# Performance work log

Measured on AMD Instinct MI355X. Metric: run time of the kernel, lower is better.

Reference implementation:

```python
import jax, jax.numpy as jnp
import numpy as np

B, T, C, H = 8, 2048, 1024, 128

def setup_inputs() -> dict:
    key = jax.random.key(0)
    k1, k2, k3, k4 = jax.random.split(key, 4)
    scale = 0.02
    return {
        "x": jax.random.normal(k1, (B, T, C), dtype=jnp.float32),
        "Wq": jax.random.normal(k2, (C, H), dtype=jnp.float32) * scale,
        "Wk": jax.random.normal(k3, (C, H), dtype=jnp.float32) * scale,
        "Wv": jax.random.normal(k4, (C, H), dtype=jnp.float32) * scale,
    }

def reference(x, Wq, Wk, Wv):
    # Single causal attention head (dropout p=0.0 -> identity)
    q = jnp.einsum('btc,ch->bth', x, Wq)
    k = jnp.einsum('btc,ch->bth', x, Wk)
    v = jnp.einsum('btc,ch->bth', x, Wv)
    head_size = k.shape[-1]
    scores = jnp.einsum('bth,bsh->bts', q, k) / jnp.sqrt(jnp.asarray(head_size, q.dtype))  # [B,T,T]
    causal = jnp.tril(jnp.ones((scores.shape[1], scores.shape[2]), dtype=bool))
    scores = jnp.where(causal, scores, -jnp.inf)
    weights = jax.nn.softmax(scores, axis=-1)
    context = jnp.einsum('bts,bsh->bth', weights, v)  # [B,T,H]
    return context
```

## Files before the change

### kernel.cpp

```cpp
#include <hip/hip_runtime.h>

typedef __bf16 bf16x8 __attribute__((ext_vector_type(8)));
typedef float f32x4 __attribute__((ext_vector_type(4)));
typedef float fv4 __attribute__((ext_vector_type(4)));

#define B_ 8
#define T_ 2048
#define C_ 1024
#define H_ 128

__global__ __launch_bounds__(256) void prep_kernel(
    const float* __restrict__ Wq, const float* __restrict__ Wk,
    const float* __restrict__ Wv, __bf16* __restrict__ Wt)
{
  __shared__ __bf16 ldsT[128 * 136];
  const int tid = threadIdx.x;
  const int k0 = blockIdx.x * 128;
  const int wsel = blockIdx.y;
  const float* W = wsel == 0 ? Wq : (wsel == 1 ? Wk : Wv);
#pragma unroll
  for (int i = 0; i < 16; ++i) {
    int fidx = tid + 256 * i;
    int k = fidx >> 5, h4 = (fidx & 31) << 2;
    fv4 w = *(const fv4*)(W + (size_t)(k0 + k) * H_ + h4);
#pragma unroll
    for (int j = 0; j < 4; ++j) ldsT[(h4 + j) * 136 + k] = (__bf16)w[j];
  }
  __syncthreads();
#pragma unroll
  for (int i = 0; i < 8; ++i) {
    int sidx = tid + 256 * i;
    int h = sidx >> 4, c8 = (sidx & 15) << 3;
    *(bf16x8*)(Wt + (size_t)wsel * H_ * C_ + (size_t)h * C_ + k0 + c8) =
        *(const bf16x8*)&ldsT[h * 136 + c8];
  }
}

__global__ __launch_bounds__(256) void proj_kernel(
    const float* __restrict__ x, const __bf16* __restrict__ Wt,
    __bf16* __restrict__ Qw, __bf16* __restrict__ Kw, __bf16* __restrict__ Vtw)
{
  __shared__ __align__(16) __bf16 ldsA[32 * 40];
  __shared__ __align__(16) __bf16 ldsB[384 * 40];
  const int tid = threadIdx.x;
  const int wave = tid >> 6, lane = tid & 63;
  const int q4 = lane >> 4, l16 = lane & 15;
  const int bt0 = blockIdx.x * 32;

  const f32x4 zero4 = {0.f, 0.f, 0.f, 0.f};
  f32x4 acc[2][6];
#pragma unroll
  for (int mt = 0; mt < 2; ++mt)
#pragma unroll
    for (int nt = 0; nt < 6; ++nt) acc[mt][nt] = zero4;

  const int arow = tid >> 2, acol8 = (tid & 3) << 3;

  fv4 xa[2][2];
  bf16x8 wp[2][6];
#pragma unroll
  for (int slot = 0; slot < 2; ++slot) {
    const int kb = slot * 32;
    if (tid < 128) {
      const float* s = x + (size_t)(bt0 + arow) * C_ + kb + acol8;
      xa[slot][0] = *(const fv4*)s;
      xa[slot][1] = *(const fv4*)(s + 4);
    }
#pragma unroll
    for (int i = 0; i < 6; ++i) {
      int idx = tid + 256 * i;
      int col = idx >> 2, k8 = (idx & 3) << 3;
      wp[slot][i] = *(const bf16x8*)(Wt + (size_t)col * C_ + kb + k8);
    }
  }

  for (int c = 0; c < 32; ++c) {
    const int s = c & 1;
    if (tid < 128) {
      bf16x8 v;
#pragma unroll
      for (int j = 0; j < 4; ++j) { v[j] = (__bf16)xa[s][0][j]; v[4 + j] = (__bf16)xa[s][1][j]; }
      *(bf16x8*)&ldsA[arow * 40 + acol8] = v;
    }
#pragma unroll
    for (int i = 0; i < 6; ++i) {
      int idx = tid + 256 * i;
      int col = idx >> 2, k8 = (idx & 3) << 3;
      *(bf16x8*)&ldsB[col * 40 + k8] = wp[s][i];
    }
    __syncthreads();
    const int kn = (c + 2 < 32) ? (c + 2) * 32 : c * 32;
    if (tid < 128) {
      const float* sp = x + (size_t)(bt0 + arow) * C_ + kn + acol8;
      xa[s][0] = *(const fv4*)sp;
      xa[s][1] = *(const fv4*)(sp + 4);
    }
#pragma unroll
    for (int i = 0; i < 6; ++i) {
      int idx = tid + 256 * i;
      int col = idx >> 2, k8 = (idx & 3) << 3;
      wp[s][i] = *(const bf16x8*)(Wt + (size_t)col * C_ + kn + k8);
    }
    bf16x8 af[2];
#pragma unroll
    for (int mt = 0; mt < 2; ++mt)
      af[mt] = *(const bf16x8*)&ldsA[(mt * 16 + l16) * 40 + q4 * 8];
#pragma unroll
    for (int nt = 0; nt < 6; ++nt) {
      bf16x8 bf = *(const bf16x8*)&ldsB[(wave * 96 + nt * 16 + l16) * 40 + q4 * 8];
#pragma unroll
      for (int mt = 0; mt < 2; ++mt)
        acc[mt][nt] = __builtin_amdgcn_mfma_f32_16x16x32_bf16(af[mt], bf, acc[mt][nt], 0, 0, 0);
    }
    __syncthreads();
  }

  const int b = bt0 >> 11, t0 = bt0 & (T_ - 1);
#pragma unroll
  for (int mt = 0; mt < 2; ++mt)
#pragma unroll
    for (int nt = 0; nt < 6; ++nt) {
      int gcol = wave * 96 + nt * 16 + l16;
#pragma unroll
      for (int r = 0; r < 4; ++r) {
        int row = bt0 + mt * 16 + q4 * 4 + r;
        float v = acc[mt][nt][r];
        if (gcol < 128) Qw[(size_t)row * H_ + gcol] = (__bf16)v;
        else if (gcol < 256) Kw[(size_t)row * H_ + (gcol - 128)] = (__bf16)v;
        else {
          int tl = mt * 16 + q4 * 4 + r;
          ldsB[(gcol - 256) * 40 + tl] = (__bf16)v;
        }
      }
    }
  __syncthreads();
#pragma unroll
  for (int i = 0; i < 2; ++i) {
    int idx = tid + 256 * i;
    int h = idx >> 2, t8 = (idx & 3) << 3;
    *(bf16x8*)(Vtw + ((size_t)b * H_ + h) * T_ + t0 + t8) =
        *(const bf16x8*)&ldsB[h * 40 + t8];
  }
}

__global__ __launch_bounds__(256) void attn_split(
    const __bf16* __restrict__ Q, const __bf16* __restrict__ K,
    const __bf16* __restrict__ Vt, __bf16* __restrict__ PO,
    float* __restrict__ Pl, float* __restrict__ out)
{
  __shared__ __align__(16) __bf16 ldsK[64 * 136];
  __shared__ __align__(16) __bf16 ldsV[128 * 72];
  __shared__ __align__(16) __bf16 ldsP[4][16 * 72];
  const int tid = threadIdx.x;
  const int wave = tid >> 6, lane = tid & 63;
  const int q4 = lane >> 4, l16 = lane & 15;
  const int b = blockIdx.y;
  int rem = blockIdx.x, qb = 0;
  while (rem >= (qb >> 3) + 1) { rem -= (qb >> 3) + 1; ++qb; }
  const int c = rem;
  const int tstart = c << 3;
  const int tend = min(tstart + 8, qb + 1);
  const int nch = (qb >> 3) + 1;
  const int qw = qb * 64 + wave * 16;
  const __bf16* Qb = Q + (size_t)b * T_ * H_;
  const __bf16* Kb = K + (size_t)b * T_ * H_;
  const __bf16* Vb = Vt + (size_t)b * H_ * T_;
  __bf16* ldsPw = &ldsP[wave][0];

  bf16x8 qf[4];
#pragma unroll
  for (int kc = 0; kc < 4; ++kc)
    qf[kc] = *(const bf16x8*)(Qb + (size_t)(qw + l16) * H_ + kc * 32 + q4 * 8);

  const f32x4 zero4 = {0.f, 0.f, 0.f, 0.f};
  f32x4 o[8];
#pragma unroll
  for (int nt = 0; nt < 8; ++nt) o[nt] = zero4;
  float lsum[4] = {0.f, 0.f, 0.f, 0.f};

  bf16x8 kp[4], vp[4];
#pragma unroll
  for (int i = 0; i < 4; ++i) {
    int idx = tid + 256 * i;
    int krow = idx >> 4, kcol8 = (idx & 15) << 3;
    kp[i] = *(const bf16x8*)(Kb + (size_t)(tstart * 64 + krow) * H_ + kcol8);
    int vrow = idx >> 3, vcol8 = (idx & 7) << 3;
    vp[i] = *(const bf16x8*)(Vb + (size_t)vrow * T_ + tstart * 64 + vcol8);
  }

  for (int t = tstart; t < tend; ++t) {
    const int kv0 = t << 6;
#pragma unroll
    for (int i = 0; i < 4; ++i) {
      int idx = tid + 256 * i;
      int krow = idx >> 4, kcol8 = (idx & 15) << 3;
      *(bf16x8*)&ldsK[krow * 136 + kcol8] = kp[i];
      int vrow = idx >> 3, vcol8 = (idx & 7) << 3;
      *(bf16x8*)&ldsV[vrow * 72 + vcol8] = vp[i];
    }
    __syncthreads();
    const int kvn = (t + 1 < tend) ? (kv0 + 64) : kv0;
#pragma unroll
    for (int i = 0; i < 4; ++i) {
      int idx = tid + 256 * i;
      int krow = idx >> 4, kcol8 = (idx & 15) << 3;
      kp[i] = *(const bf16x8*)(Kb + (size_t)(kvn + krow) * H_ + kcol8);
      int vrow = idx >> 3, vcol8 = (idx & 7) << 3;
      vp[i] = *(const bf16x8*)(Vb + (size_t)vrow * T_ + kvn + vcol8);
    }

    f32x4 s[4];
#pragma unroll
    for (int nt = 0; nt < 4; ++nt) s[nt] = zero4;
#pragma unroll
    for (int nt = 0; nt < 4; ++nt)
#pragma unroll
      for (int kc = 0; kc < 4; ++kc) {
        bf16x8 kf = *(const bf16x8*)&ldsK[(nt * 16 + l16) * 136 + kc * 32 + q4 * 8];
        s[nt] = __builtin_amdgcn_mfma_f32_16x16x32_bf16(qf[kc], kf, s[nt], 0, 0, 0);
      }

    if (t == qb) {
#pragma unroll
      for (int r = 0; r < 4; ++r) {
        const int grow = qw + q4 * 4 + r;
#pragma unroll
        for (int nt = 0; nt < 4; ++nt) {
          int col = kv0 + nt * 16 + l16;
          float p = (col <= grow) ? __expf(s[nt][r] * 0.08838834764831845f) : 0.f;
          lsum[r] += p;
          ldsPw[(q4 * 4 + r) * 72 + nt * 16 + l16] = (__bf16)p;
        }
      }
    } else {
#pragma unroll
      for (int r = 0; r < 4; ++r)
#pragma unroll
        for (int nt = 0; nt < 4; ++nt) {
          float p = __expf(s[nt][r] * 0.08838834764831845f);
          lsum[r] += p;
          ldsPw[(q4 * 4 + r) * 72 + nt * 16 + l16] = (__bf16)p;
        }
    }
#pragma unroll
    for (int kc2 = 0; kc2 < 2; ++kc2) {
      bf16x8 pf = *(const bf16x8*)&ldsPw[l16 * 72 + kc2 * 32 + q4 * 8];
#pragma unroll
      for (int nt = 0; nt < 8; ++nt) {
        bf16x8 vf = *(const bf16x8*)&ldsV[(nt * 16 + l16) * 72 + kc2 * 32 + q4 * 8];
        o[nt] = __builtin_amdgcn_mfma_f32_16x16x32_bf16(pf, vf, o[nt], 0, 0, 0);
      }
    }
    __syncthreads();
  }

  float lred[4];
#pragma unroll
  for (int r = 0; r < 4; ++r) {
    float l = lsum[r];
    l += __shfl_xor(l, 1);
    l += __shfl_xor(l, 2);
    l += __shfl_xor(l, 4);
    l += __shfl_xor(l, 8);
    lred[r] = l;
  }

  if (nch == 1) {
#pragma unroll
    for (int r = 0; r < 4; ++r) lred[r] = 1.f / lred[r];
#pragma unroll
    for (int nt = 0; nt < 8; ++nt)
#pragma unroll
      for (int r = 0; r < 4; ++r) {
        int row = qw + q4 * 4 + r;
        out[((size_t)b * T_ + row) * H_ + nt * 16 + l16] = o[nt][r] * lred[r];
      }
  } else {
    const int slot = b * 80 + qb + max(qb - 8, 0) + max(qb - 16, 0) + max(qb - 24, 0) + c;
    __bf16* POs = PO + (size_t)slot * 8192;
#pragma unroll
    for (int nt = 0; nt < 8; ++nt)
#pragma unroll
      for (int r = 0; r < 4; ++r)
        POs[(wave * 16 + q4 * 4 + r) * 128 + nt * 16 + l16] = (__bf16)o[nt][r];
    if (l16 == 0)
#pragma unroll
      for (int r = 0; r < 4; ++r)
        Pl[slot * 64 + wave * 16 + q4 * 4 + r] = lred[r];
  }
}

__global__ __launch_bounds__(256) void attn_combine(
    const __bf16* __restrict__ PO, const float* __restrict__ Pl,
    float* __restrict__ out)
{
  const int qb = 8 + (blockIdx.x >> 2);
  const int seg = blockIdx.x & 3;
  const int b = blockIdx.y;
  const int nch = (qb >> 3) + 1;
  const int slot0 = b * 80 + qb + max(qb - 8, 0) + max(qb - 16, 0) + max(qb - 24, 0);
  const int tid = threadIdx.x;
  const int rloc = seg * 16 + (tid >> 4);
  const int col8 = (tid & 15) << 3;
  float oacc[8] = {0.f};
  float lacc = 0.f;
  for (int cc = 0; cc < nch; ++cc) {
    const int slot = slot0 + cc;
    lacc += Pl[slot * 64 + rloc];
    bf16x8 v = *(const bf16x8*)(PO + (size_t)slot * 8192 + rloc * 128 + col8);
#pragma unroll
    for (int j = 0; j < 8; ++j) oacc[j] += (float)v[j];
  }
  const float inv = 1.f / lacc;
  float* op = out + ((size_t)b * T_ + qb * 64 + rloc) * H_ + col8;
  fv4 v0, v1;
#pragma unroll
  for (int j = 0; j < 4; ++j) { v0[j] = oacc[j] * inv; v1[j] = oacc[4 + j] * inv; }
  *(fv4*)op = v0;
  *(fv4*)(op + 4) = v1;
}

__global__ __launch_bounds__(256) void attn_mono(
    const __bf16* __restrict__ Q, const __bf16* __restrict__ K,
    const __bf16* __restrict__ Vt, float* __restrict__ out)
{
  __shared__ __align__(16) __bf16 ldsK[64 * 136];
  __shared__ __align__(16) __bf16 ldsV[128 * 72];
  __shared__ __align__(16) __bf16 ldsP[4][16 * 72];
  const int tid = threadIdx.x;
  const int wave = tid >> 6, lane = tid & 63;
  const int q4 = lane >> 4, l16 = lane & 15;
  const int qb = blockIdx.x, b = blockIdx.y;
  const int qw = qb * 64 + wave * 16;
  const __bf16* Qb = Q + (size_t)b * T_ * H_;
  const __bf16* Kb = K + (size_t)b * T_ * H_;
  const __bf16* Vb = Vt + (size_t)b * H_ * T_;
  __bf16* ldsPw = &ldsP[wave][0];

  bf16x8 qf[4];
#pragma unroll
  for (int kc = 0; kc < 4; ++kc)
    qf[kc] = *(const bf16x8*)(Qb + (size_t)(qw + l16) * H_ + kc * 32 + q4 * 8);

  const f32x4 zero4 = {0.f, 0.f, 0.f, 0.f};
  f32x4 o[8];
#pragma unroll
  for (int nt = 0; nt < 8; ++nt) o[nt] = zero4;
  float lsum[4] = {0.f, 0.f, 0.f, 0.f};
  const int ntile = qb + 1;

  bf16x8 kp[4], vp[4];
#pragma unroll
  for (int i = 0; i < 4; ++i) {
    int idx = tid + 256 * i;
    int krow = idx >> 4, kcol8 = (idx & 15) << 3;
    kp[i] = *(const bf16x8*)(Kb + (size_t)krow * H_ + kcol8);
    int vrow = idx >> 3, vcol8 = (idx & 7) << 3;
    vp[i] = *(const bf16x8*)(Vb + (size_t)vrow * T_ + vcol8);
  }

  for (int t = 0; t < ntile; ++t) {
    const int kv0 = t << 6;
#pragma unroll
    for (int i = 0; i < 4; ++i) {
      int idx = tid + 256 * i;
      int krow = idx >> 4, kcol8 = (idx & 15) << 3;
      *(bf16x8*)&ldsK[krow * 136 + kcol8] = kp[i];
      int vrow = idx >> 3, vcol8 = (idx & 7) << 3;
      *(bf16x8*)&ldsV[vrow * 72 + vcol8] = vp[i];
    }
    __syncthreads();
    int kvn = (t + 1 < ntile) ? (kv0 + 64) : kv0;
#pragma unroll
    for (int i = 0; i < 4; ++i) {
      int idx = tid + 256 * i;
      int krow = idx >> 4, kcol8 = (idx & 15) << 3;
      kp[i] = *(const bf16x8*)(Kb + (size_t)(kvn + krow) * H_ + kcol8);
      int vrow = idx >> 3, vcol8 = (idx & 7) << 3;
      vp[i] = *(const bf16x8*)(Vb + (size_t)vrow * T_ + kvn + vcol8);
    }
    f32x4 s[4];
#pragma unroll
    for (int nt = 0; nt < 4; ++nt) s[nt] = zero4;
#pragma unroll
    for (int nt = 0; nt < 4; ++nt)
#pragma unroll
      for (int kc = 0; kc < 4; ++kc) {
        bf16x8 kf = *(const bf16x8*)&ldsK[(nt * 16 + l16) * 136 + kc * 32 + q4 * 8];
        s[nt] = __builtin_amdgcn_mfma_f32_16x16x32_bf16(qf[kc], kf, s[nt], 0, 0, 0);
      }
#pragma unroll
    for (int r = 0; r < 4; ++r) {
      const int grow = qw + q4 * 4 + r;
#pragma unroll
      for (int nt = 0; nt < 4; ++nt) {
        int col = kv0 + nt * 16 + l16;
        float p = (col <= grow) ? __expf(s[nt][r] * 0.08838834764831845f) : 0.f;
        lsum[r] += p;
        ldsPw[(q4 * 4 + r) * 72 + nt * 16 + l16] = (__bf16)p;
      }
    }
#pragma unroll
    for (int kc2 = 0; kc2 < 2; ++kc2) {
      bf16x8 pf = *(const bf16x8*)&ldsPw[l16 * 72 + kc2 * 32 + q4 * 8];
#pragma unroll
      for (int nt = 0; nt < 8; ++nt) {
        bf16x8 vf = *(const bf16x8*)&ldsV[(nt * 16 + l16) * 72 + kc2 * 32 + q4 * 8];
        o[nt] = __builtin_amdgcn_mfma_f32_16x16x32_bf16(pf, vf, o[nt], 0, 0, 0);
      }
    }
    __syncthreads();
  }
  float rinv[4];
#pragma unroll
  for (int r = 0; r < 4; ++r) {
    float l = lsum[r];
    l += __shfl_xor(l, 1);
    l += __shfl_xor(l, 2);
    l += __shfl_xor(l, 4);
    l += __shfl_xor(l, 8);
    rinv[r] = 1.f / l;
  }
#pragma unroll
  for (int nt = 0; nt < 8; ++nt)
#pragma unroll
    for (int r = 0; r < 4; ++r) {
      int row = qw + q4 * 4 + r;
      out[((size_t)b * T_ + row) * H_ + nt * 16 + l16] = o[nt][r] * rinv[r];
    }
}

extern "C" void kernel_launch(void* const* d_in, const int* in_sizes, int n_in,
                              void* d_out, int out_size, void* d_ws, size_t ws_size,
                              hipStream_t stream) {
  const float* x  = (const float*)d_in[0];
  const float* Wq = (const float*)d_in[1];
  const float* Wk = (const float*)d_in[2];
  const float* Wv = (const float*)d_in[3];
  __bf16* ws = (__bf16*)d_ws;
  __bf16* Qw  = ws;
  __bf16* Kw  = ws + (size_t)B_ * T_ * H_;
  __bf16* Vtw = ws + (size_t)2 * B_ * T_ * H_;
  __bf16* Wt  = ws + (size_t)3 * B_ * T_ * H_;
  const size_t bf16_elems = 6684672;
  __bf16* PO = ws + bf16_elems;
  float* Pl = (float*)(ws + bf16_elems + (size_t)640 * 8192);
  const size_t need = bf16_elems * 2 + (size_t)640 * 8192 * 2 + (size_t)640 * 64 * 4;
  float* out = (float*)d_out;

  prep_kernel<<<dim3(8, 3), 256, 0, stream>>>(Wq, Wk, Wv, Wt);
  proj_kernel<<<512, 256, 0, stream>>>(x, Wt, Qw, Kw, Vtw);
  if (ws_size >= need) {
    attn_split<<<dim3(80, 8), 256, 0, stream>>>(Qw, Kw, Vtw, PO, Pl, out);
    attn_combine<<<dim3(96, 8), 256, 0, stream>>>(PO, Pl, out);
  } else {
    attn_mono<<<dim3(32, 8), 256, 0, stream>>>(Qw, Kw, Vtw, out);
  }
}
```

Baseline: 170.3 us.

## Rewrite QKV projection with direct global-to-LDS loads, swizzled tiles, 2D grid

The projection GEMM now stages x (as fp32) and the transposed weights straight into double-buffered, XOR-swizzled LDS tiles using global_load_lds, so data no longer passes through registers. The tile grows to 64 rows by 192 columns with a 2x2 wave layout over a 256x2 grid, and the K step grows to 64. The fp32-to-bf16 conversion of x moves into the LDS read path. The aim is less register pressure and staging overhead plus better load/compute overlap. The cost is more LDS per block, and because each block covers only half the 384 columns, every x tile is now fetched by two blocks.

```diff
diff --git a/kernel.cpp b/kernel.cpp
--- a/kernel.cpp
+++ b/kernel.cpp
@@ -8,6 +8,12 @@
 #define T_ 2048
 #define C_ 1024
 #define H_ 128
+
+__device__ __forceinline__ void gload16(void* lds, const void* g) {
+  __builtin_amdgcn_global_load_lds(
+      (const __attribute__((address_space(1))) void*)g,
+      (__attribute__((address_space(3))) void*)lds, 16, 0, 0);
+}
 
 __global__ __launch_bounds__(256) void prep_kernel(
     const float* __restrict__ Wq, const float* __restrict__ Wk,
@@ -40,12 +46,17 @@
     const float* __restrict__ x, const __bf16* __restrict__ Wt,
     __bf16* __restrict__ Qw, __bf16* __restrict__ Kw, __bf16* __restrict__ Vtw)
 {
-  __shared__ __align__(16) __bf16 ldsA[32 * 40];
-  __shared__ __align__(16) __bf16 ldsB[384 * 40];
+  __shared__ __align__(16) float ldsA[2][64 * 64];
+  __shared__ __align__(16) __bf16 ldsB[2][192 * 64];
   const int tid = threadIdx.x;
   const int wave = tid >> 6, lane = tid & 63;
   const int q4 = lane >> 4, l16 = lane & 15;
-  const int bt0 = blockIdx.x * 32;
+  const int wm = wave >> 1, wn = wave & 1;
+  const int bt0 = blockIdx.x * 64;
+  const int cb0 = blockIdx.y * 192;
+
+  const int arow16 = tid >> 4, agx = tid & 15;
+  const int bcol32 = tid >> 3, bgx = tid & 7;
 
   const f32x4 zero4 = {0.f, 0.f, 0.f, 0.f};
   f32x4 acc[2][6];
@@ -54,92 +65,76 @@
 #pragma unroll
     for (int nt = 0; nt < 6; ++nt) acc[mt][nt] = zero4;
 
-  const int arow = tid >> 2, acol8 = (tid & 3) << 3;
-
-  fv4 xa[2][2];
-  bf16x8 wp[2][6];
-#pragma unroll
-  for (int slot = 0; slot < 2; ++slot) {
-    const int kb = slot * 32;
-    if (tid < 128) {
-      const float* s = x + (size_t)(bt0 + arow) * C_ + kb + acol8;
-      xa[slot][0] = *(const fv4*)s;
-      xa[slot][1] = *(const fv4*)(s + 4);
+  auto stage = [&](int bufi, int k0) {
+#pragma unroll
+    for (int i = 0; i < 4; ++i) {
+      int row = i * 16 + arow16;
+      gload16((char*)&ldsA[bufi][0] + i * 4096 + wave * 1024,
+              x + (size_t)(bt0 + row) * C_ + k0 + ((agx ^ (row & 7)) << 2));
     }
 #pragma unroll
     for (int i = 0; i < 6; ++i) {
+      int col = i * 32 + bcol32;
+      gload16((char*)&ldsB[bufi][0] + i * 4096 + wave * 1024,
+              Wt + (size_t)(cb0 + col) * C_ + k0 + ((bgx ^ (col & 7)) << 3));
+    }
+  };
+
+  stage(0, 0);
+  __syncthreads();
+
+  for (int it = 0; it < 16; ++it) {
+    const int buf = it & 1;
+    if (it + 1 < 16) stage(buf ^ 1, (it + 1) * 64);
+#pragma unroll
+    for (int kc = 0; kc < 2; ++kc) {
+      bf16x8 af[2];
+#pragma unroll
+      for (int mt = 0; mt < 2; ++mt) {
+        const int rl = wm * 32 + mt * 16 + l16;
+        const int rx = rl & 7;
+        fv4 a0 = *(const fv4*)&ldsA[buf][rl * 64 + (((kc * 8 + q4 * 2 + 0) ^ rx) << 2)];
+        fv4 a1 = *(const fv4*)&ldsA[buf][rl * 64 + (((kc * 8 + q4 * 2 + 1) ^ rx) << 2)];
+#pragma unroll
+        for (int j = 0; j < 4; ++j) { af[mt][j] = (__bf16)a0[j]; af[mt][4 + j] = (__bf16)a1[j]; }
+      }
+#pragma unroll
+      for (int nt = 0; nt < 6; ++nt) {
+        const int cl = wn * 96 + nt * 16 + l16;
+        bf16x8 bf = *(const bf16x8*)&ldsB[buf][cl * 64 + (((kc * 4 + q4) ^ (cl & 7)) << 3)];
+#pragma unroll
+        for (int mt = 0; mt < 2; ++mt)
+          acc[mt][nt] = __builtin_amdgcn_mfma_f32_16x16x32_bf16(af[mt], bf, acc[mt][nt], 0, 0, 0);
+      }
+    }
+    __syncthreads();
+  }
+
+  const int b = bt0 >> 11, t0 = bt0 & (T_ - 1);
+  __bf16* ldsV = (__bf16*)&ldsB[0][0];
+#pragma unroll
+  for (int mt = 0; mt < 2; ++mt)
+#pragma unroll
+    for (int nt = 0; nt < 6; ++nt) {
+      int gcol = cb0 + wn * 96 + nt * 16 + l16;
+#pragma unroll
+      for (int r = 0; r < 4; ++r) {
+        int tl = wm * 32 + mt * 16 + q4 * 4 + r;
+        float v = acc[mt][nt][r];
+        if (gcol < 128) Qw[(size_t)(bt0 + tl) * H_ + gcol] = (__bf16)v;
+        else if (gcol < 256) Kw[(size_t)(bt0 + tl) * H_ + (gcol - 128)] = (__bf16)v;
+        else ldsV[(gcol - 256) * 72 + tl] = (__bf16)v;
+      }
+    }
+  if (cb0 == 192) {
+    __syncthreads();
+#pragma unroll
+    for (int i = 0; i < 4; ++i) {
       int idx = tid + 256 * i;
-      int col = idx >> 2, k8 = (idx & 3) << 3;
-      wp[slot][i] = *(const bf16x8*)(Wt + (size_t)col * C_ + kb + k8);
-    }
-  }
-
-  for (int c = 0; c < 32; ++c) {
-    const int s = c & 1;
-    if (tid < 128) {
-      bf16x8 v;
-#pragma unroll
-      for (int j = 0; j < 4; ++j) { v[j] = (__bf16)xa[s][0][j]; v[4 + j] = (__bf16)xa[s][1][j]; }
-      *(bf16x8*)&ldsA[arow * 40 + acol8] = v;
-    }
-#pragma unroll
-    for (int i = 0; i < 6; ++i) {
-      int idx = tid + 256 * i;
-      int col = idx >> 2, k8 = (idx & 3) << 3;
-      *(bf16x8*)&ldsB[col * 40 + k8] = wp[s][i];
-    }
-    __syncthreads();
-    const int kn = (c + 2 < 32) ? (c + 2) * 32 : c * 32;
-    if (tid < 128) {
-      const float* sp = x + (size_t)(bt0 + arow) * C_ + kn + acol8;
-      xa[s][0] = *(const fv4*)sp;
-      xa[s][1] = *(const fv4*)(sp + 4);
-    }
-#pragma unroll
-    for (int i = 0; i < 6; ++i) {
-      int idx = tid + 256 * i;
-      int col = idx >> 2, k8 = (idx & 3) << 3;
-      wp[s][i] = *(const bf16x8*)(Wt + (size_t)col * C_ + kn + k8);
-    }
-    bf16x8 af[2];
-#pragma unroll
-    for (int mt = 0; mt < 2; ++mt)
-      af[mt] = *(const bf16x8*)&ldsA[(mt * 16 + l16) * 40 + q4 * 8];
-#pragma unroll
-    for (int nt = 0; nt < 6; ++nt) {
-      bf16x8 bf = *(const bf16x8*)&ldsB[(wave * 96 + nt * 16 + l16) * 40 + q4 * 8];
-#pragma unroll
-      for (int mt = 0; mt < 2; ++mt)
-        acc[mt][nt] = __builtin_amdgcn_mfma_f32_16x16x32_bf16(af[mt], bf, acc[mt][nt], 0, 0, 0);
-    }
-    __syncthreads();
-  }
-
-  const int b = bt0 >> 11, t0 = bt0 & (T_ - 1);
-#pragma unroll
-  for (int mt = 0; mt < 2; ++mt)
-#pragma unroll
-    for (int nt = 0; nt < 6; ++nt) {
-      int gcol = wave * 96 + nt * 16 + l16;
-#pragma unroll
-      for (int r = 0; r < 4; ++r) {
-        int row = bt0 + mt * 16 + q4 * 4 + r;
-        float v = acc[mt][nt][r];
-        if (gcol < 128) Qw[(size_t)row * H_ + gcol] = (__bf16)v;
-        else if (gcol < 256) Kw[(size_t)row * H_ + (gcol - 128)] = (__bf16)v;
-        else {
-          int tl = mt * 16 + q4 * 4 + r;
-          ldsB[(gcol - 256) * 40 + tl] = (__bf16)v;
-        }
-      }
-    }
-  __syncthreads();
-#pragma unroll
-  for (int i = 0; i < 2; ++i) {
-    int idx = tid + 256 * i;
-    int h = idx >> 2, t8 = (idx & 3) << 3;
-    *(bf16x8*)(Vtw + ((size_t)b * H_ + h) * T_ + t0 + t8) =
-        *(const bf16x8*)&ldsB[h * 40 + t8];
+      int h = idx >> 3, t8 = (idx & 7) << 3;
+      *(bf16x8*)(Vtw + ((size_t)b * H_ + h) * T_ + t0 + t8) =
+          *(const bf16x8*)&ldsV[h * 72 + t8];
+    }
   }
 }
 
@@ -449,7 +444,7 @@
   float* out = (float*)d_out;
 
   prep_kernel<<<dim3(8, 3), 256, 0, stream>>>(Wq, Wk, Wv, Wt);
-  proj_kernel<<<512, 256, 0, stream>>>(x, Wt, Qw, Kw, Vtw);
+  proj_kernel<<<dim3(256, 2), 256, 0, stream>>>(x, Wt, Qw, Kw, Vtw);
   if (ws_size >= need) {
     attn_split<<<dim3(80, 8), 256, 0, stream>>>(Qw, Kw, Vtw, PO, Pl, out);
     attn_combine<<<dim3(96, 8), 256, 0, stream>>>(PO, Pl, out);
```

New measurement: 157.1 us. -7.8%, faster.
